# Kernel optimization log

Hardware: AMD Instinct MI355X
Metric: run time of the kernel (lower is better)

The kernel has to match this reference:

```python
import jax, jax.numpy as jnp
import numpy as np

BN_EPS = 1e-5


def setup_inputs() -> dict:
    key = jax.random.key(0)
    k1, k2, k3 = jax.random.split(key, 3)
    B, IN, H, C = 65536, 784, 1024, 10
    x = jax.random.normal(k1, (B, IN), dtype=jnp.float32)
    # Kaiming-ish real-valued latent weights
    w1 = jax.random.normal(k2, (H, IN), dtype=jnp.float32) * 0.03
    w2 = jax.random.normal(k3, (C, H), dtype=jnp.float32) * 0.03
    gamma = jnp.ones((H,), dtype=jnp.float32)
    beta = jnp.zeros((H,), dtype=jnp.float32)
    return {"x": x, "w1": w1, "w2": w2, "gamma": gamma, "beta": beta}


def _bin_weight(w):
    # XNOR-Net weight binarization: per-output-row alpha * sign(w)
    alpha = jnp.mean(jnp.abs(w), axis=1, keepdims=True)  # [out, 1]
    return alpha * jnp.sign(w)


def reference(x, w1, w2, gamma, beta):
    x = x.reshape(x.shape[0], -1)                      # [B, 784]
    h = x @ _bin_weight(w1).T                          # [B, 1024]
    # BatchNorm1d, training mode: batch mean / biased variance
    mu = jnp.mean(h, axis=0)
    var = jnp.mean(jnp.square(h - mu), axis=0)
    h = gamma * (h - mu) * jax.lax.rsqrt(var + BN_EPS) + beta
    a = jnp.sign(h)                                    # binarized activation
    out = a @ _bin_weight(w2).T                        # [B, 10]
    return out
```

## Files before the change

kernel.cpp:

```cpp
#include <hip/hip_runtime.h>
#include <hip/hip_fp16.h>

#define BATCH   65536
#define IN_DIM  784
#define KH      800
#define NSTEP   25
#define H_DIM   1024
#define C_DIM   10
#define BN_EPS  1e-5f
#define SLOTH   16384

typedef _Float16 half8 __attribute__((ext_vector_type(8)));
typedef float    f32x4 __attribute__((ext_vector_type(4)));

#if defined(__has_builtin)
#if __has_builtin(__builtin_amdgcn_global_load_lds)
#define HAVE_ASYNC 1
#endif
#endif
#ifndef HAVE_ASYNC
#define HAVE_ASYNC 0
#endif

__device__ __forceinline__ void stage16(const _Float16* g, _Float16* ldsBase, int lane) {
#if HAVE_ASYNC
  __builtin_amdgcn_global_load_lds((const __attribute__((address_space(1))) void*)g,
                                   (__attribute__((address_space(3))) void*)ldsBase,
                                   16, 0, 0);
#else
  *(half8*)(ldsBase + lane * 8) = *(const half8*)g;
#endif
}

__global__ __launch_bounds__(256) void prep_w(const float* __restrict__ w1,
                                              const float* __restrict__ w2,
                                              float* __restrict__ alpha1,
                                              _Float16* __restrict__ S2,
                                              _Float16* __restrict__ S2W,
                                              float* __restrict__ A2P,
                                              float* __restrict__ colz) {
  __shared__ float red[4];
  const int tid = threadIdx.x, lane = tid & 63, wave = tid >> 6;
  const int j = blockIdx.x;
  if (j < H_DIM) {
    const float* wr = w1 + (long)j * IN_DIM;
    float s = 0.f;
    for (int k = tid; k < IN_DIM; k += 256) s += fabsf(wr[k]);
#pragma unroll
    for (int off = 32; off > 0; off >>= 1) s += __shfl_xor(s, off, 64);
    if (lane == 0) red[wave] = s;
    __syncthreads();
    if (tid == 0) alpha1[j] = (red[0] + red[1] + red[2] + red[3]) * (1.f / IN_DIM);
    _Float16* dr = S2 + (long)j * KH;
    for (int k = tid; k < KH; k += 256) {
      const float v = (k < IN_DIM) ? wr[k] : 0.f;
      dr[k] = (_Float16)((v > 0.f) ? 1.f : ((v < 0.f) ? -1.f : 0.f));
    }
  } else if (j < H_DIM + C_DIM) {
    const int c = j - H_DIM;
    const float* wr = w2 + (long)c * H_DIM;
    float s = 0.f;
    for (int k = tid; k < H_DIM; k += 256) s += fabsf(wr[k]);
#pragma unroll
    for (int off = 32; off > 0; off >>= 1) s += __shfl_xor(s, off, 64);
    if (lane == 0) red[wave] = s;
    __syncthreads();
    if (tid == 0) A2P[c] = (red[0] + red[1] + red[2] + red[3]) * (1.f / H_DIM);
    for (int k = tid; k < H_DIM; k += 256) {
      const float v = wr[k];
      S2W[(long)c * H_DIM + k] = (_Float16)((v > 0.f) ? 1.f : ((v < 0.f) ? -1.f : 0.f));
    }
  } else {
    for (int k = tid; k < 2 * H_DIM; k += 256) colz[k] = 0.f;
    for (int k = tid; k < 6 * H_DIM; k += 256) S2W[10 * H_DIM + k] = (_Float16)0.f;
    if (tid < 6) A2P[10 + tid] = 0.f;
  }
}

__global__ __launch_bounds__(512, 4) void gemm1(const float* __restrict__ x,
                                                const _Float16* __restrict__ S2,
                                                const float* __restrict__ alpha1,
                                                float* __restrict__ H,
                                                float* __restrict__ colsum,
                                                float* __restrict__ colsumsq) {
  __shared__ _Float16 lds[2 * SLOTH];
  const int tid  = threadIdx.x;
  const int lane = tid & 63;
  const int w    = tid >> 6;
  const int wr   = w >> 2;
  const int wc   = w & 3;

  const int b     = blockIdx.x;
  const int xcd   = b & 7;
  const int local = b >> 3;
  const long m0   = (long)(xcd * 64 + (local >> 2)) * 128;
  const int  n0   = (local & 3) * 256;

  const int rowS = tid >> 2;
  const int q    = tid & 3;
  const float* xp = x + (m0 + rowS) * (long)IN_DIM;
  const int cq = (q ^ ((rowS >> 1) & 3)) * 8;
  const int aw = rowS * 32;

  const int c8 = ((lane & 3) ^ ((lane >> 3) & 3)) * 8;
  const _Float16* bG = S2 + (long)(n0 + w * 32 + (lane >> 2)) * KH + c8;
  const int ldsW0 = (w * 32) * 32;
  const int ldsW1 = (w * 32 + 16) * 32;

  const int fr = lane & 15;
  const int kc = lane >> 4;
  const int cp = (kc ^ ((fr >> 1) & 3)) * 8;
  const int aoff = (wr * 64 + fr) * 32 + cp;
  const int boff = (wc * 64 + fr) * 32 + cp;

  f32x4 acc[4][4] = {};

#define ALOAD(R0, R1, KB) do {                                               \
    if (((KB) + q * 8) <= (IN_DIM - 8)) {                                    \
      const float* src = xp + (KB) + q * 8;                                  \
      (R0) = *(const f32x4*)(src);                                           \
      (R1) = *(const f32x4*)(src + 4);                                       \
    } else { (R0) = f32x4{}; (R1) = f32x4{}; }                               \
  } while (0)

#define CONV_WRITE(R0, R1, PW, KB) do {                                      \
    half8 hh = {}, hl = {};                                                  \
    if (((KB) + q * 8) <= (IN_DIM - 8)) {                                    \
      _Pragma("unroll")                                                      \
      for (int i = 0; i < 8; ++i) {                                          \
        const float f = (i < 4) ? (R0)[i] : (R1)[i & 3];                     \
        const _Float16 h = (_Float16)f;                                      \
        hh[i] = h; hl[i] = (_Float16)(f - (float)h);                         \
      }                                                                      \
    }                                                                        \
    *(half8*)((PW) + aw + cq) = hh;                                          \
    *(half8*)((PW) + 4096 + aw + cq) = hl;                                   \
  } while (0)

  stage16(bG + 0,           lds + 8192 + ldsW0, lane);
  stage16(bG + 16 * KH + 0, lds + 8192 + ldsW1, lane);
  {
    f32x4 r0, r1;
    ALOAD(r0, r1, 0);
    asm volatile("s_waitcnt vmcnt(0)" ::: "memory");
    CONV_WRITE(r0, r1, (&lds[0]), 0);
  }

  for (int t = 0; t < NSTEP; ++t) {
    _Float16* Scur = &lds[(t & 1) * SLOTH];
    _Float16* Pw   = &lds[((t + 1) & 1) * SLOTH];
    const int kb = ((t + 1 < NSTEP) ? (t + 1) : (NSTEP - 1)) * 32;

    asm volatile("s_waitcnt lgkmcnt(0)" ::: "memory");
    __builtin_amdgcn_s_barrier();
    asm volatile("" ::: "memory");

    stage16(bG + kb,           Pw + 8192 + ldsW0, lane);
    stage16(bG + 16 * KH + kb, Pw + 8192 + ldsW1, lane);
    f32x4 r0, r1;
    ALOAD(r0, r1, kb);

    half8 af[4], bf[4];
#pragma unroll
    for (int ni = 0; ni < 4; ++ni) bf[ni] = *(const half8*)&Scur[8192 + boff + ni * 512];
#pragma unroll
    for (int mi = 0; mi < 4; ++mi) af[mi] = *(const half8*)&Scur[aoff + mi * 512];
    __builtin_amdgcn_s_setprio(1);
#pragma unroll
    for (int mi = 0; mi < 4; ++mi)
#pragma unroll
      for (int ni = 0; ni < 4; ++ni)
        acc[mi][ni] = __builtin_amdgcn_mfma_f32_16x16x32_f16(af[mi], bf[ni], acc[mi][ni], 0, 0, 0);
    __builtin_amdgcn_s_setprio(0);
#pragma unroll
    for (int mi = 0; mi < 4; ++mi) af[mi] = *(const half8*)&Scur[4096 + aoff + mi * 512];
    __builtin_amdgcn_s_setprio(1);
#pragma unroll
    for (int mi = 0; mi < 4; ++mi)
#pragma unroll
      for (int ni = 0; ni < 4; ++ni)
        acc[mi][ni] = __builtin_amdgcn_mfma_f32_16x16x32_f16(af[mi], bf[ni], acc[mi][ni], 0, 0, 0);
    __builtin_amdgcn_s_setprio(0);

    asm volatile("s_waitcnt vmcnt(0)" ::: "memory");
    CONV_WRITE(r0, r1, Pw, kb);
  }

  asm volatile("s_waitcnt vmcnt(0)" ::: "memory");

  const int rq = (lane >> 4) * 4;
#pragma unroll
  for (int ni = 0; ni < 4; ++ni) {
    const int col = n0 + wc * 64 + ni * 16 + fr;
    const float a1 = alpha1[col];
    float s = 0.f, qq = 0.f;
#pragma unroll
    for (int mi = 0; mi < 4; ++mi) {
#pragma unroll
      for (int r = 0; r < 4; ++r) {
        const long row = m0 + wr * 64 + mi * 16 + rq + r;
        const float v = acc[mi][ni][r] * a1;
        H[row * H_DIM + col] = v;
        s += v;
        qq += v * v;
      }
    }
    s += __shfl_xor(s, 16, 64);
    s += __shfl_xor(s, 32, 64);
    qq += __shfl_xor(qq, 16, 64);
    qq += __shfl_xor(qq, 32, 64);
    if ((lane >> 4) == 0) {
      atomicAdd(&colsum[col], s);
      atomicAdd(&colsumsq[col], qq);
    }
  }
#undef ALOAD
#undef CONV_WRITE
}

__global__ __launch_bounds__(256) void final_k(const float* __restrict__ H,
                                               const float* __restrict__ colsum,
                                               const float* __restrict__ colsumsq,
                                               const float* __restrict__ gamma,
                                               const float* __restrict__ beta,
                                               const _Float16* __restrict__ S2W,
                                               const float* __restrict__ A2P,
                                               float* __restrict__ out) {
  __shared__ _Float16 bs[16 * H_DIM];
  __shared__ float cs[H_DIM], ts[H_DIM];
  const int tid = threadIdx.x, lane = tid & 63, wave = tid >> 6;

  {
    const int j = tid * 4;
    const f32x4 s  = *(const f32x4*)&colsum[j];
    const f32x4 q  = *(const f32x4*)&colsumsq[j];
    const f32x4 g  = *(const f32x4*)&gamma[j];
    const f32x4 bt = *(const f32x4*)&beta[j];
    f32x4 c, t;
#pragma unroll
    for (int i = 0; i < 4; ++i) {
      const float mu  = s[i] * (1.f / BATCH);
      const float var = q[i] * (1.f / BATCH) - mu * mu;
      c[i] = g[i] * rsqrtf(var + BN_EPS);
      t[i] = bt[i] - c[i] * mu;
    }
    *(f32x4*)&cs[j] = c;
    *(f32x4*)&ts[j] = t;
  }
  for (int i = tid; i < 2048; i += 256) {
    const int oc = i >> 7, cc = i & 127;
    *(half8*)&bs[oc * H_DIM + ((cc ^ (oc & 7)) << 3)] = *(const half8*)&S2W[oc * H_DIM + (cc << 3)];
  }
  __syncthreads();

  const int lr = lane & 15, lg = lane >> 4;
  const float alf = A2P[lr];
  const long r0 = ((long)blockIdx.x * 4 + wave) * 16;
  const float* hp = H + (r0 + lr) * H_DIM + lg * 8;

  f32x4 acc = {};
#pragma unroll 4
  for (int ks = 0; ks < 32; ++ks) {
    const f32x4 h0 = *(const f32x4*)(hp + ks * 32);
    const f32x4 h1 = *(const f32x4*)(hp + ks * 32 + 4);
    const int jb = ks * 32 + lg * 8;
    const f32x4 c0v = *(const f32x4*)&cs[jb];
    const f32x4 c1v = *(const f32x4*)&cs[jb + 4];
    const f32x4 t0v = *(const f32x4*)&ts[jb];
    const f32x4 t1v = *(const f32x4*)&ts[jb + 4];
    half8 afr;
#pragma unroll
    for (int i = 0; i < 4; ++i) {
      const float hv = h0[i] * c0v[i] + t0v[i];
      afr[i] = (_Float16)((hv > 0.f) ? 1.f : ((hv < 0.f) ? -1.f : 0.f));
    }
#pragma unroll
    for (int i = 0; i < 4; ++i) {
      const float hv = h1[i] * c1v[i] + t1v[i];
      afr[4 + i] = (_Float16)((hv > 0.f) ? 1.f : ((hv < 0.f) ? -1.f : 0.f));
    }
    const int cc = (ks * 4 + lg) ^ (lr & 7);
    const half8 bfr = *(const half8*)&bs[lr * H_DIM + cc * 8];
    acc = __builtin_amdgcn_mfma_f32_16x16x32_f16(afr, bfr, acc, 0, 0, 0);
  }

  __syncthreads();
  float* outs = (float*)bs;
  if (lr < C_DIM) {
#pragma unroll
    for (int r = 0; r < 4; ++r)
      outs[(wave * 16 + lg * 4 + r) * C_DIM + lr] = acc[r] * alf;
  }
  __syncthreads();
  if (tid < 160)
    *(f32x4*)&out[(long)blockIdx.x * 640 + tid * 4] = *(const f32x4*)&outs[tid * 4];
}

extern "C" void kernel_launch(void* const* d_in, const int* in_sizes, int n_in,
                              void* d_out, int out_size, void* d_ws, size_t ws_size,
                              hipStream_t stream) {
  const float* x     = (const float*)d_in[0];
  const float* w1    = (const float*)d_in[1];
  const float* w2    = (const float*)d_in[2];
  const float* gamma = (const float*)d_in[3];
  const float* beta  = (const float*)d_in[4];
  float* out = (float*)d_out;

  char* ws = (char*)d_ws;
  float*    H      = (float*)   (ws + 0);
  _Float16* S2     = (_Float16*)(ws + 268435456LL);
  _Float16* S2W    = (_Float16*)(ws + 270073856LL);
  float*    ALPHA1 = (float*)   (ws + 270106624LL);
  float*    A2P    = (float*)   (ws + 270110720LL);
  float*    COLS   = (float*)   (ws + 270110976LL);
  float*    COLQ   = (float*)   (ws + 270115072LL);

  prep_w<<<H_DIM + C_DIM + 1, 256, 0, stream>>>(w1, w2, ALPHA1, S2, S2W, A2P, COLS);
  gemm1<<<2048, 512, 0, stream>>>(x, S2, ALPHA1, H, COLS, COLQ);
  final_k<<<BATCH / 64, 256, 0, stream>>>(H, COLS, COLQ, gamma, beta, S2W, A2P, out);
}
```

Before: 534.3 us.

## Stage fp32 x tiles asynchronously into LDS and split to fp16 hi/lo per wave

The x tile is now loaded with async global-to-LDS copies as raw fp32 (swizzled), like the weight tile, instead of through registers with a blocking convert-and-store before the barrier. Each wave converts its own fragment to hi/lo fp16 just before the MFMAs. The wave tiling changes from 2x4 (64x64 per wave) to 4x2 (32x128 per wave), so each wave loads 8 B fragments and 2 A fragments. This removes the register round trip and a vmcnt stall from the pipeline. In exchange the fp32-to-fp16 split is recomputed by every wave that reads a row, and the K-tail padding now relies on redirected pointers rather than explicit zero-filling.

New measurement: 568.8 us. 1.06x slower.

```diff
diff --git a/kernel.cpp b/kernel.cpp
--- a/kernel.cpp
+++ b/kernel.cpp
@@ -22,13 +22,13 @@
 #define HAVE_ASYNC 0
 #endif
 
-__device__ __forceinline__ void stage16(const _Float16* g, _Float16* ldsBase, int lane) {
+__device__ __forceinline__ void stage16(const void* g, void* ldsBase, int lane) {
 #if HAVE_ASYNC
   __builtin_amdgcn_global_load_lds((const __attribute__((address_space(1))) void*)g,
                                    (__attribute__((address_space(3))) void*)ldsBase,
                                    16, 0, 0);
 #else
-  *(half8*)(ldsBase + lane * 8) = *(const half8*)g;
+  *(half8*)((_Float16*)ldsBase + lane * 8) = *(const half8*)((const _Float16*)g + lane * 8);
 #endif
 }
 
@@ -87,8 +87,8 @@
   const int tid  = threadIdx.x;
   const int lane = tid & 63;
   const int w    = tid >> 6;
-  const int wr   = w >> 2;
-  const int wc   = w & 3;
+  const int wrr  = w & 3;
+  const int wcc  = w >> 2;
 
   const int b     = blockIdx.x;
   const int xcd   = b & 7;
@@ -96,11 +96,14 @@
   const long m0   = (long)(xcd * 64 + (local >> 2)) * 128;
   const int  n0   = (local & 3) * 256;
 
-  const int rowS = tid >> 2;
-  const int q    = tid & 3;
-  const float* xp = x + (m0 + rowS) * (long)IN_DIM;
-  const int cq = (q ^ ((rowS >> 1) & 3)) * 8;
-  const int aw = rowS * 32;
+  const int s0  = (w * 2) * 64 + lane;
+  const int s1  = s0 + 64;
+  const int ar0 = s0 >> 3, ac0 = ((s0 & 7) ^ (ar0 & 7)) * 4;
+  const int ar1 = s1 >> 3, ac1 = ((s1 & 7) ^ (ar1 & 7)) * 4;
+  const float* aG0 = x + (m0 + ar0) * (long)IN_DIM + ac0;
+  const float* aG1 = x + (m0 + ar1) * (long)IN_DIM + ac1;
+  const float* aG0p = (768 + ac0 + 4 <= IN_DIM) ? aG0 : (x + (m0 + ar0) * (long)IN_DIM);
+  const float* aG1p = (768 + ac1 + 4 <= IN_DIM) ? aG1 : (x + (m0 + ar1) * (long)IN_DIM);
 
   const int c8 = ((lane & 3) ^ ((lane >> 3) & 3)) * 8;
   const _Float16* bG = S2 + (long)(n0 + w * 32 + (lane >> 2)) * KH + c8;
@@ -109,96 +112,78 @@
 
   const int fr = lane & 15;
   const int kc = lane >> 4;
-  const int cp = (kc ^ ((fr >> 1) & 3)) * 8;
-  const int aoff = (wr * 64 + fr) * 32 + cp;
-  const int boff = (wc * 64 + fr) * 32 + cp;
-
-  f32x4 acc[4][4] = {};
-
-#define ALOAD(R0, R1, KB) do {                                               \
-    if (((KB) + q * 8) <= (IN_DIM - 8)) {                                    \
-      const float* src = xp + (KB) + q * 8;                                  \
-      (R0) = *(const f32x4*)(src);                                           \
-      (R1) = *(const f32x4*)(src + 4);                                       \
-    } else { (R0) = f32x4{}; (R1) = f32x4{}; }                               \
-  } while (0)
-
-#define CONV_WRITE(R0, R1, PW, KB) do {                                      \
-    half8 hh = {}, hl = {};                                                  \
-    if (((KB) + q * 8) <= (IN_DIM - 8)) {                                    \
-      _Pragma("unroll")                                                      \
-      for (int i = 0; i < 8; ++i) {                                          \
-        const float f = (i < 4) ? (R0)[i] : (R1)[i & 3];                     \
-        const _Float16 h = (_Float16)f;                                      \
-        hh[i] = h; hl[i] = (_Float16)(f - (float)h);                         \
-      }                                                                      \
-    }                                                                        \
-    *(half8*)((PW) + aw + cq) = hh;                                          \
-    *(half8*)((PW) + 4096 + aw + cq) = hl;                                   \
-  } while (0)
-
-  stage16(bG + 0,           lds + 8192 + ldsW0, lane);
-  stage16(bG + 16 * KH + 0, lds + 8192 + ldsW1, lane);
-  {
-    f32x4 r0, r1;
-    ALOAD(r0, r1, 0);
-    asm volatile("s_waitcnt vmcnt(0)" ::: "memory");
-    CONV_WRITE(r0, r1, (&lds[0]), 0);
-  }
+  const int cp   = (kc ^ ((fr >> 1) & 3)) * 8;
+  const int boff = (wcc * 128 + fr) * 32 + cp;
+  const int aF   = (wrr * 32 + fr) * 32;
+  const int aC0  = ((2 * kc) ^ (fr & 7)) * 4;
+  const int aC1  = ((2 * kc + 1) ^ (fr & 7)) * 4;
+
+  f32x4 acc[2][8] = {};
+
+  stage16(aG0, lds + (w * 2) * 512, lane);
+  stage16(aG1, lds + (w * 2 + 1) * 512, lane);
+  stage16(bG,           lds + 8192 + ldsW0, lane);
+  stage16(bG + 16 * KH, lds + 8192 + ldsW1, lane);
 
   for (int t = 0; t < NSTEP; ++t) {
     _Float16* Scur = &lds[(t & 1) * SLOTH];
     _Float16* Pw   = &lds[((t + 1) & 1) * SLOTH];
-    const int kb = ((t + 1 < NSTEP) ? (t + 1) : (NSTEP - 1)) * 32;
-
-    asm volatile("s_waitcnt lgkmcnt(0)" ::: "memory");
+    const int kbn  = ((t + 1 < NSTEP) ? (t + 1) : (NSTEP - 1)) * 32;
+    const bool pad = (kbn == 768);
+
+    asm volatile("s_waitcnt vmcnt(0)" ::: "memory");
     __builtin_amdgcn_s_barrier();
     asm volatile("" ::: "memory");
 
-    stage16(bG + kb,           Pw + 8192 + ldsW0, lane);
-    stage16(bG + 16 * KH + kb, Pw + 8192 + ldsW1, lane);
-    f32x4 r0, r1;
-    ALOAD(r0, r1, kb);
-
-    half8 af[4], bf[4];
-#pragma unroll
-    for (int ni = 0; ni < 4; ++ni) bf[ni] = *(const half8*)&Scur[8192 + boff + ni * 512];
-#pragma unroll
-    for (int mi = 0; mi < 4; ++mi) af[mi] = *(const half8*)&Scur[aoff + mi * 512];
-    __builtin_amdgcn_s_setprio(1);
-#pragma unroll
-    for (int mi = 0; mi < 4; ++mi)
-#pragma unroll
-      for (int ni = 0; ni < 4; ++ni)
-        acc[mi][ni] = __builtin_amdgcn_mfma_f32_16x16x32_f16(af[mi], bf[ni], acc[mi][ni], 0, 0, 0);
-    __builtin_amdgcn_s_setprio(0);
-#pragma unroll
-    for (int mi = 0; mi < 4; ++mi) af[mi] = *(const half8*)&Scur[4096 + aoff + mi * 512];
-    __builtin_amdgcn_s_setprio(1);
-#pragma unroll
-    for (int mi = 0; mi < 4; ++mi)
-#pragma unroll
-      for (int ni = 0; ni < 4; ++ni)
-        acc[mi][ni] = __builtin_amdgcn_mfma_f32_16x16x32_f16(af[mi], bf[ni], acc[mi][ni], 0, 0, 0);
-    __builtin_amdgcn_s_setprio(0);
-
-    asm volatile("s_waitcnt vmcnt(0)" ::: "memory");
-    CONV_WRITE(r0, r1, Pw, kb);
+    stage16((pad ? aG0p : aG0) + kbn, Pw + (w * 2) * 512, lane);
+    stage16((pad ? aG1p : aG1) + kbn, Pw + (w * 2 + 1) * 512, lane);
+    stage16(bG + kbn,           Pw + 8192 + ldsW0, lane);
+    stage16(bG + 16 * KH + kbn, Pw + 8192 + ldsW1, lane);
+
+    half8 bf[8];
+#pragma unroll
+    for (int ni = 0; ni < 8; ++ni) bf[ni] = *(const half8*)&Scur[8192 + boff + ni * 512];
+
+    const float* Af = (const float*)Scur;
+#pragma unroll
+    for (int mi = 0; mi < 2; ++mi) {
+      const f32x4 r0 = *(const f32x4*)&Af[aF + mi * 512 + aC0];
+      const f32x4 r1 = *(const f32x4*)&Af[aF + mi * 512 + aC1];
+      half8 ah, al;
+#pragma unroll
+      for (int i = 0; i < 4; ++i) {
+        const _Float16 h = (_Float16)r0[i];
+        ah[i] = h; al[i] = (_Float16)(r0[i] - (float)h);
+      }
+#pragma unroll
+      for (int i = 0; i < 4; ++i) {
+        const _Float16 h = (_Float16)r1[i];
+        ah[4 + i] = h; al[4 + i] = (_Float16)(r1[i] - (float)h);
+      }
+      __builtin_amdgcn_s_setprio(1);
+#pragma unroll
+      for (int ni = 0; ni < 8; ++ni)
+        acc[mi][ni] = __builtin_amdgcn_mfma_f32_16x16x32_f16(ah, bf[ni], acc[mi][ni], 0, 0, 0);
+#pragma unroll
+      for (int ni = 0; ni < 8; ++ni)
+        acc[mi][ni] = __builtin_amdgcn_mfma_f32_16x16x32_f16(al, bf[ni], acc[mi][ni], 0, 0, 0);
+      __builtin_amdgcn_s_setprio(0);
+    }
   }
 
   asm volatile("s_waitcnt vmcnt(0)" ::: "memory");
 
   const int rq = (lane >> 4) * 4;
 #pragma unroll
-  for (int ni = 0; ni < 4; ++ni) {
-    const int col = n0 + wc * 64 + ni * 16 + fr;
+  for (int ni = 0; ni < 8; ++ni) {
+    const int col = n0 + wcc * 128 + ni * 16 + fr;
     const float a1 = alpha1[col];
     float s = 0.f, qq = 0.f;
 #pragma unroll
-    for (int mi = 0; mi < 4; ++mi) {
+    for (int mi = 0; mi < 2; ++mi) {
 #pragma unroll
       for (int r = 0; r < 4; ++r) {
-        const long row = m0 + wr * 64 + mi * 16 + rq + r;
+        const long row = m0 + wrr * 32 + mi * 16 + rq + r;
         const float v = acc[mi][ni][r] * a1;
         H[row * H_DIM + col] = v;
         s += v;
@@ -214,8 +199,6 @@
       atomicAdd(&colsumsq[col], qq);
     }
   }
-#undef ALOAD
-#undef CONV_WRITE
 }
 
 __global__ __launch_bounds__(256) void final_k(const float* __restrict__ H,
```
